# Kernel optimization log

Measured on AMD Instinct MI355X. Metric: run time of the kernel, lower is better.

## Reference

```python
import jax, jax.numpy as jnp
import numpy as np

NUM_HEADS = 8

def setup_inputs() -> dict:
    key = jax.random.key(0)
    ks = jax.random.split(key, 7)
    B, Cin, H, W = 4, 256, 56, 56
    Cout = 256
    s = 1.0 / np.sqrt(Cin)
    return {
        "x": jax.random.normal(ks[0], (B, Cin, H, W), dtype=jnp.float32),
        "wq": jax.random.normal(ks[1], (Cout, Cin), dtype=jnp.float32) * s,
        "bq": jax.random.normal(ks[2], (Cout,), dtype=jnp.float32) * s,
        "wk": jax.random.normal(ks[3], (Cout, Cin), dtype=jnp.float32) * s,
        "bk": jax.random.normal(ks[4], (Cout,), dtype=jnp.float32) * s,
        "wv": jax.random.normal(ks[5], (Cout, Cin), dtype=jnp.float32) * s,
        "bv": jax.random.normal(ks[6], (Cout,), dtype=jnp.float32) * s,
    }

def _proj(x, w, b):
    # 1x1 conv == per-pixel linear: [B,Cin,H,W] x [Cout,Cin] -> [B,Cout,H,W]
    return jnp.einsum('bchw,oc->bohw', x, w) + b[None, :, None, None]

def reference(x, wq, bq, wk, bk, wv, bv):
    B, _, H, W = x.shape
    Cout = wq.shape[0]
    hd = Cout // NUM_HEADS
    N = H * W
    # project and reshape to [B, heads, N, head_dim]
    def split_heads(t):
        return t.reshape(B, NUM_HEADS, hd, N).transpose(0, 1, 3, 2)
    q = split_heads(_proj(x, wq, bq))
    k = split_heads(_proj(x, wk, bk))
    v = split_heads(_proj(x, wv, bv))
    scores = jnp.einsum('bhnd,bhmd->bhnm', q, k) / jnp.sqrt(jnp.float32(hd))
    attn = jax.nn.softmax(scores, axis=-1)          # [B, heads, N, N]
    out = jnp.einsum('bhnm,bhmd->bhnd', attn, v)    # [B, heads, N, hd]
    out = out.transpose(0, 1, 3, 2).reshape(B, Cout, H, W)
    return out
```

## Files before the change

kernel.cpp:

```cpp
#include <hip/hip_runtime.h>
#include <math.h>


#define NB   4
#define CIN  256
#define NPIX 3136
#define NH   8
#define HD   32
#define QSC  0.25503837897544295f

typedef float          f32x4  __attribute__((ext_vector_type(4)));
typedef short          bf16x8 __attribute__((ext_vector_type(8)));
typedef unsigned int   u32x4  __attribute__((ext_vector_type(4)));
typedef unsigned int   u32x2  __attribute__((ext_vector_type(2)));
typedef unsigned short u16x4  __attribute__((ext_vector_type(4)));

static __device__ __forceinline__ unsigned short f2bf(float f) {
  union { float f; unsigned u; } v; v.f = f;
  return (unsigned short)((v.u + 0x7fffu + ((v.u >> 16) & 1u)) >> 16);
}

static __device__ __forceinline__ float fast_exp2(float x) {
#if __has_builtin(__builtin_amdgcn_exp2f)
  return __builtin_amdgcn_exp2f(x);
#else
  return exp2f(x);
#endif
}

static __device__ __forceinline__ unsigned cvt_pk_bf16(float lo, float hi) {
  unsigned r;
  asm("v_cvt_pk_bf16_f32 %0, %1, %2" : "=v"(r) : "v"(lo), "v"(hi));
  return r;
}

static __device__ __forceinline__ void gload_lds16(const void* g, void* l) {
  __builtin_amdgcn_global_load_lds(
      (__attribute__((address_space(1))) const void*)g,
      (__attribute__((address_space(3))) void*)l, 16, 0, 0);
}

static __device__ __forceinline__ bf16x8 lds_frag16(const unsigned char* p) {
  u32x4 u = *(const u32x4*)p;
  return __builtin_bit_cast(bf16x8, u);
}

__global__ __launch_bounds__(256) void k_xpose(const float* __restrict__ x,
                                               unsigned short* __restrict__ xbT) {
  __shared__ unsigned short tile[64][66];
  const int n0 = blockIdx.x * 64, c0 = blockIdx.y * 64, b = blockIdx.z;
  const int t = threadIdx.x;
  const int cl = t >> 4, nl = (t & 15) * 4;
#pragma unroll
  for (int rep = 0; rep < 4; ++rep) {
    const int c = cl + rep * 16;
    f32x4 v = *(const f32x4*)(x + ((size_t)(b * CIN + c0 + c)) * NPIX + n0 + nl);
    tile[nl + 0][c] = f2bf(v.x);
    tile[nl + 1][c] = f2bf(v.y);
    tile[nl + 2][c] = f2bf(v.z);
    tile[nl + 3][c] = f2bf(v.w);
  }
  __syncthreads();
  const int nr = t >> 2, co = (t & 3) * 16;
  unsigned pw[8];
#pragma unroll
  for (int j = 0; j < 8; ++j)
    pw[j] = (unsigned)tile[nr][co + 2 * j] | ((unsigned)tile[nr][co + 2 * j + 1] << 16);
  unsigned short* dst = xbT + ((size_t)(b * NPIX + n0 + nr)) * 256 + c0 + co;
  u32x4 lo = {pw[0], pw[1], pw[2], pw[3]};
  u32x4 hi = {pw[4], pw[5], pw[6], pw[7]};
  *(u32x4*)dst = lo;
  *(u32x4*)(dst + 8) = hi;
}

__global__ __launch_bounds__(256) void k_wconv(const float* __restrict__ wq,
                                               const float* __restrict__ wk,
                                               const float* __restrict__ wv,
                                               unsigned short* __restrict__ wb) {
  const int i = blockIdx.x * 256 + threadIdx.x;
  const int mat = i >> 16, idx = i & 65535;
  const float* w = (mat == 0) ? wq : (mat == 1 ? wk : wv);
  const float s = (mat == 0) ? QSC : 1.0f;
  wb[i] = f2bf(w[idx] * s);
}

__global__ __launch_bounds__(256) void k_proj(
    const unsigned short* __restrict__ xbT, const unsigned short* __restrict__ wb,
    const float* __restrict__ bq, const float* __restrict__ bk,
    const float* __restrict__ bv,
    unsigned short* __restrict__ qws, unsigned short* __restrict__ kws,
    unsigned short* __restrict__ vtws) {
  __shared__ alignas(16) unsigned char lds[20480];
  const int b = blockIdx.y & 3, mat = blockIdx.y >> 2;
  const int n0 = blockIdx.x * 64;
  const int t = threadIdx.x, l = t & 63, wid = t >> 6, g = l >> 4, q = l & 15;
  const unsigned short* wmat = wb + mat * (256 * 256);

  f32x4 acc[4][4] = {};

  for (int ks = 0; ks < 8; ++ks) {
#pragma unroll
    for (int r = 0; r < 4; ++r) {
      const unsigned short* src = wmat + ((wid + 4 * r) * 16 + q) * 256 + ks * 32 + g * 8;
      gload_lds16(src, lds + (r * 256 + t) * 16);
    }
    gload_lds16(xbT + ((size_t)(b * NPIX + n0 + wid * 16 + q)) * 256 + ks * 32 + g * 8,
                lds + 16384 + t * 16);
    __syncthreads();

    bf16x8 wa[4], xf[4];
#pragma unroll
    for (int r = 0; r < 4; ++r) wa[r] = lds_frag16(lds + (r * 256 + wid * 64 + l) * 16);
#pragma unroll
    for (int nt = 0; nt < 4; ++nt) xf[nt] = lds_frag16(lds + 16384 + (nt * 64 + l) * 16);
#pragma unroll
    for (int r = 0; r < 4; ++r)
#pragma unroll
      for (int nt = 0; nt < 4; ++nt)
        acc[r][nt] = __builtin_amdgcn_mfma_f32_16x16x32_bf16(wa[r], xf[nt], acc[r][nt], 0, 0, 0);
    __syncthreads();
  }

  const float* bias = (mat == 0) ? bq : (mat == 1 ? bk : bv);
  const float bsc = (mat == 0) ? QSC : 1.0f;
#pragma unroll
  for (int r = 0; r < 4; ++r) {
    const int ob = (wid + 4 * r) * 16 + g * 4;
    const int h = ob >> 5, d0 = ob & 31;
    const float b0 = bias[ob + 0] * bsc, b1 = bias[ob + 1] * bsc;
    const float b2 = bias[ob + 2] * bsc, b3 = bias[ob + 3] * bsc;
#pragma unroll
    for (int nt = 0; nt < 4; ++nt) {
      const int n = n0 + nt * 16 + q;
      f32x4 a = acc[r][nt];
      if (mat < 2) {
        unsigned short* dst = (mat == 0) ? qws : kws;
        u16x4 pk = {f2bf(a.x + b0), f2bf(a.y + b1), f2bf(a.z + b2), f2bf(a.w + b3)};
        *(u16x4*)(dst + ((size_t)((b * NH + h) * NPIX + n)) * HD + d0) = pk;
      } else {
        unsigned short* vr = vtws + ((size_t)((b * NH + h) * HD + d0)) * NPIX + n;
        vr[0] = f2bf(a.x + b0);
        vr[(size_t)NPIX] = f2bf(a.y + b1);
        vr[(size_t)2 * NPIX] = f2bf(a.z + b2);
        vr[(size_t)3 * NPIX] = f2bf(a.w + b3);
      }
    }
  }
}

__global__ __launch_bounds__(256) void k_attn(
    const unsigned short* __restrict__ qws, const unsigned short* __restrict__ kws,
    const unsigned short* __restrict__ vtws, float* __restrict__ out) {
  __shared__ alignas(16) unsigned char lds[24576];
  const int bh = blockIdx.y;
  const int q0 = blockIdx.x * 64;
  const int t = threadIdx.x, l = t & 63, wid = t >> 6, g = l >> 4, q = l & 15;

  u32x4 qu = *(const u32x4*)(qws + ((size_t)(bh * NPIX + q0 + wid * 16 + q)) * HD + g * 8);
  const bf16x8 qf = __builtin_bit_cast(bf16x8, qu);
  const f32x4 zero4 = {0.f, 0.f, 0.f, 0.f};

  float lsum = 0.0f;
  f32x4 oacc0 = zero4;
  f32x4 oacc1 = zero4;

  const unsigned short* ksrc = kws + ((size_t)(bh * NPIX + wid * 16 + q)) * HD + g * 8;
  const unsigned short* vsrc =
      vtws + ((size_t)(bh * HD + (wid >> 1) * 16 + q)) * NPIX + (wid & 1) * 32 + g * 8;

  unsigned bofs = 0;
  gload_lds16(ksrc, lds + t * 16);
  gload_lds16(vsrc, lds + 4096 + t * 16);
  __syncthreads();

  for (int kt = 0; kt < 49; ++kt) {
    if (kt < 48) {
      gload_lds16(ksrc + (size_t)(kt + 1) * 64 * HD, lds + (bofs ^ 8192) + t * 16);
      gload_lds16(vsrc + (kt + 1) * 64, lds + (bofs ^ 8192) + 4096 + t * 16);
    }
    const unsigned char* kb = lds + bofs;
    const unsigned char* vb = lds + bofs + 4096;

    f32x4 s[4];
#pragma unroll
    for (int jj = 0; jj < 4; ++jj) {
      bf16x8 kf = lds_frag16(kb + (jj * 64 + l) * 16);
      s[jj] = __builtin_amdgcn_mfma_f32_16x16x32_bf16(kf, qf, zero4, 0, 0, 0);
    }

    float psum = 0.0f;
    unsigned pw[8];
#pragma unroll
    for (int jj = 0; jj < 4; ++jj) {
#pragma unroll
      for (int rp = 0; rp < 2; ++rp) {
        float p0 = fast_exp2(s[jj][2 * rp + 0]);
        float p1 = fast_exp2(s[jj][2 * rp + 1]);
        psum += p0 + p1;
        pw[jj * 2 + rp] = cvt_pk_bf16(p0, p1);
      }
    }
    lsum += psum;

    {
      u32x4 c0 = {pw[0], pw[1], pw[2], pw[3]};
      u32x4 c1 = {pw[4], pw[5], pw[6], pw[7]};
      *(u32x4*)(lds + 16384 + wid * 2048 + l * 16) = c0;
      *(u32x4*)(lds + 16384 + wid * 2048 + 1024 + l * 16) = c1;
    }

#pragma unroll
    for (int c = 0; c < 2; ++c) {
      const unsigned char* pbase = lds + 16384 + wid * 2048 + c * 1024 + q * 16 + (g & 2) * 4;
      u32x2 plo = *(const u32x2*)(pbase + ((2 * g) & 3) * 256);
      u32x2 phi = *(const u32x2*)(pbase + ((2 * g + 1) & 3) * 256);
      u32x4 pu = {plo.x, plo.y, phi.x, phi.y};
      bf16x8 pf = __builtin_bit_cast(bf16x8, pu);
      bf16x8 v0 = lds_frag16(vb + (c * 64 + l) * 16);
      bf16x8 v1 = lds_frag16(vb + (128 + c * 64 + l) * 16);
      oacc0 = __builtin_amdgcn_mfma_f32_16x16x32_bf16(v0, pf, oacc0, 0, 0, 0);
      oacc1 = __builtin_amdgcn_mfma_f32_16x16x32_bf16(v1, pf, oacc1, 0, 0, 0);
    }

    __syncthreads();
    bofs ^= 8192;
  }

  lsum += __shfl_xor(lsum, 16, 64);
  lsum += __shfl_xor(lsum, 32, 64);
  const float inv = 1.0f / lsum;

  float* ob = out + (size_t)(bh * HD) * NPIX + q0 + wid * 16 + q;
#pragma unroll
  for (int r = 0; r < 4; ++r) {
    ob[(size_t)(g * 4 + r) * NPIX] = oacc0[r] * inv;
    ob[(size_t)(16 + g * 4 + r) * NPIX] = oacc1[r] * inv;
  }
}

extern "C" void kernel_launch(void* const* d_in, const int* in_sizes, int n_in,
                              void* d_out, int out_size, void* d_ws, size_t ws_size,
                              hipStream_t stream) {
  const float* x  = (const float*)d_in[0];
  const float* wq = (const float*)d_in[1];
  const float* bq = (const float*)d_in[2];
  const float* wk = (const float*)d_in[3];
  const float* bk = (const float*)d_in[4];
  const float* wv = (const float*)d_in[5];
  const float* bv = (const float*)d_in[6];
  float* out = (float*)d_out;

  unsigned char* ws = (unsigned char*)d_ws;
  unsigned short* xbT  = (unsigned short*)(ws);
  unsigned short* wb   = (unsigned short*)(ws + 6422528);
  unsigned short* qws  = (unsigned short*)(ws + 6815744);
  unsigned short* kws  = (unsigned short*)(ws + 13238272);
  unsigned short* vtws = (unsigned short*)(ws + 19660800);

  k_xpose<<<dim3(49, 4, 4), 256, 0, stream>>>(x, xbT);
  k_wconv<<<dim3(768), 256, 0, stream>>>(wq, wk, wv, wb);
  k_proj<<<dim3(49, 12), 256, 0, stream>>>(xbT, wb, bq, bk, bv, qws, kws, vtws);
  k_attn<<<dim3(49, 32), 256, 0, stream>>>(qws, kws, vtws, out);
}
```

Baseline: 117.4 us.

## Process two query tiles per wave to reuse K/V loads across 128 queries

Each attention block now handles 128 queries instead of 64, with each wave computing two 16-query tiles against the same K and V fragments loaded into LDS. This halves the K/V global-to-LDS traffic and per-tile synchronization relative to the compute, and the grid shrinks from 49 to 25 blocks per head. It also adds s_setprio around the MFMA groups and an explicit LDS wait plus scheduling barrier. The cost is more registers and LDS per block, fewer blocks (1.6k -> 800), and wasted work on the padded last tile, which relies on bounds checks.

```diff
diff --git a/kernel.cpp b/kernel.cpp
--- a/kernel.cpp
+++ b/kernel.cpp
@@ -151,22 +151,31 @@
 __global__ __launch_bounds__(256) void k_attn(
     const unsigned short* __restrict__ qws, const unsigned short* __restrict__ kws,
     const unsigned short* __restrict__ vtws, float* __restrict__ out) {
-  __shared__ alignas(16) unsigned char lds[24576];
+  __shared__ alignas(16) unsigned char lds[32768];
   const int bh = blockIdx.y;
-  const int q0 = blockIdx.x * 64;
+  const int q0 = blockIdx.x * 128;
   const int t = threadIdx.x, l = t & 63, wid = t >> 6, g = l >> 4, q = l & 15;
 
-  u32x4 qu = *(const u32x4*)(qws + ((size_t)(bh * NPIX + q0 + wid * 16 + q)) * HD + g * 8);
-  const bf16x8 qf = __builtin_bit_cast(bf16x8, qu);
+  const int nA = q0 + wid * 32 + q;
+  const int nB = nA + 16;
+  const int rowA = (nA < NPIX) ? nA : (NPIX - 1);
+  const int rowB = (nB < NPIX) ? nB : (NPIX - 1);
+
+  u32x4 quA = *(const u32x4*)(qws + ((size_t)(bh * NPIX + rowA)) * HD + g * 8);
+  u32x4 quB = *(const u32x4*)(qws + ((size_t)(bh * NPIX + rowB)) * HD + g * 8);
+  const bf16x8 qfA = __builtin_bit_cast(bf16x8, quA);
+  const bf16x8 qfB = __builtin_bit_cast(bf16x8, quB);
   const f32x4 zero4 = {0.f, 0.f, 0.f, 0.f};
 
-  float lsum = 0.0f;
-  f32x4 oacc0 = zero4;
-  f32x4 oacc1 = zero4;
+  float lsumA = 0.0f, lsumB = 0.0f;
+  f32x4 oA0 = zero4, oA1 = zero4, oB0 = zero4, oB1 = zero4;
 
   const unsigned short* ksrc = kws + ((size_t)(bh * NPIX + wid * 16 + q)) * HD + g * 8;
   const unsigned short* vsrc =
       vtws + ((size_t)(bh * HD + (wid >> 1) * 16 + q)) * NPIX + (wid & 1) * 32 + g * 8;
+
+  unsigned char* const pbaseA = lds + 16384 + wid * 4096;
+  unsigned char* const pbaseB = pbaseA + 2048;
 
   unsigned bofs = 0;
   gload_lds16(ksrc, lds + t * 16);
@@ -181,60 +190,109 @@
     const unsigned char* kb = lds + bofs;
     const unsigned char* vb = lds + bofs + 4096;
 
-    f32x4 s[4];
+    f32x4 sA[4], sB[4];
+    __builtin_amdgcn_s_setprio(1);
 #pragma unroll
     for (int jj = 0; jj < 4; ++jj) {
       bf16x8 kf = lds_frag16(kb + (jj * 64 + l) * 16);
-      s[jj] = __builtin_amdgcn_mfma_f32_16x16x32_bf16(kf, qf, zero4, 0, 0, 0);
-    }
-
-    float psum = 0.0f;
-    unsigned pw[8];
-#pragma unroll
-    for (int jj = 0; jj < 4; ++jj) {
-#pragma unroll
-      for (int rp = 0; rp < 2; ++rp) {
-        float p0 = fast_exp2(s[jj][2 * rp + 0]);
-        float p1 = fast_exp2(s[jj][2 * rp + 1]);
-        psum += p0 + p1;
-        pw[jj * 2 + rp] = cvt_pk_bf16(p0, p1);
+      sA[jj] = __builtin_amdgcn_mfma_f32_16x16x32_bf16(kf, qfA, zero4, 0, 0, 0);
+      sB[jj] = __builtin_amdgcn_mfma_f32_16x16x32_bf16(kf, qfB, zero4, 0, 0, 0);
+    }
+    __builtin_amdgcn_s_setprio(0);
+
+    {
+      float ps = 0.0f;
+      unsigned pw[8];
+#pragma unroll
+      for (int jj = 0; jj < 4; ++jj) {
+#pragma unroll
+        for (int rp = 0; rp < 2; ++rp) {
+          float p0 = fast_exp2(sA[jj][2 * rp + 0]);
+          float p1 = fast_exp2(sA[jj][2 * rp + 1]);
+          ps += p0 + p1;
+          pw[jj * 2 + rp] = cvt_pk_bf16(p0, p1);
+        }
       }
-    }
-    lsum += psum;
-
-    {
+      lsumA += ps;
       u32x4 c0 = {pw[0], pw[1], pw[2], pw[3]};
       u32x4 c1 = {pw[4], pw[5], pw[6], pw[7]};
-      *(u32x4*)(lds + 16384 + wid * 2048 + l * 16) = c0;
-      *(u32x4*)(lds + 16384 + wid * 2048 + 1024 + l * 16) = c1;
-    }
+      *(u32x4*)(pbaseA + l * 16) = c0;
+      *(u32x4*)(pbaseA + 1024 + l * 16) = c1;
+    }
+    {
+      float ps = 0.0f;
+      unsigned pw[8];
+#pragma unroll
+      for (int jj = 0; jj < 4; ++jj) {
+#pragma unroll
+        for (int rp = 0; rp < 2; ++rp) {
+          float p0 = fast_exp2(sB[jj][2 * rp + 0]);
+          float p1 = fast_exp2(sB[jj][2 * rp + 1]);
+          ps += p0 + p1;
+          pw[jj * 2 + rp] = cvt_pk_bf16(p0, p1);
+        }
+      }
+      lsumB += ps;
+      u32x4 c0 = {pw[0], pw[1], pw[2], pw[3]};
+      u32x4 c1 = {pw[4], pw[5], pw[6], pw[7]};
+      *(u32x4*)(pbaseB + l * 16) = c0;
+      *(u32x4*)(pbaseB + 1024 + l * 16) = c1;
+    }
+
+    asm volatile("s_waitcnt lgkmcnt(0)" ::: "memory");
+    __builtin_amdgcn_sched_barrier(0);
 
 #pragma unroll
     for (int c = 0; c < 2; ++c) {
-      const unsigned char* pbase = lds + 16384 + wid * 2048 + c * 1024 + q * 16 + (g & 2) * 4;
-      u32x2 plo = *(const u32x2*)(pbase + ((2 * g) & 3) * 256);
-      u32x2 phi = *(const u32x2*)(pbase + ((2 * g + 1) & 3) * 256);
-      u32x4 pu = {plo.x, plo.y, phi.x, phi.y};
-      bf16x8 pf = __builtin_bit_cast(bf16x8, pu);
       bf16x8 v0 = lds_frag16(vb + (c * 64 + l) * 16);
       bf16x8 v1 = lds_frag16(vb + (128 + c * 64 + l) * 16);
-      oacc0 = __builtin_amdgcn_mfma_f32_16x16x32_bf16(v0, pf, oacc0, 0, 0, 0);
-      oacc1 = __builtin_amdgcn_mfma_f32_16x16x32_bf16(v1, pf, oacc1, 0, 0, 0);
+
+      const unsigned char* pA = pbaseA + c * 1024 + q * 16 + (g & 2) * 4;
+      u32x2 alo = *(const u32x2*)(pA + ((2 * g) & 3) * 256);
+      u32x2 ahi = *(const u32x2*)(pA + ((2 * g + 1) & 3) * 256);
+      u32x4 au = {alo.x, alo.y, ahi.x, ahi.y};
+      bf16x8 pfA = __builtin_bit_cast(bf16x8, au);
+
+      const unsigned char* pB = pbaseB + c * 1024 + q * 16 + (g & 2) * 4;
+      u32x2 blo = *(const u32x2*)(pB + ((2 * g) & 3) * 256);
+      u32x2 bhi = *(const u32x2*)(pB + ((2 * g + 1) & 3) * 256);
+      u32x4 bu = {blo.x, blo.y, bhi.x, bhi.y};
+      bf16x8 pfB = __builtin_bit_cast(bf16x8, bu);
+
+      __builtin_amdgcn_s_setprio(1);
+      oA0 = __builtin_amdgcn_mfma_f32_16x16x32_bf16(v0, pfA, oA0, 0, 0, 0);
+      oA1 = __builtin_amdgcn_mfma_f32_16x16x32_bf16(v1, pfA, oA1, 0, 0, 0);
+      oB0 = __builtin_amdgcn_mfma_f32_16x16x32_bf16(v0, pfB, oB0, 0, 0, 0);
+      oB1 = __builtin_amdgcn_mfma_f32_16x16x32_bf16(v1, pfB, oB1, 0, 0, 0);
+      __builtin_amdgcn_s_setprio(0);
     }
 
     __syncthreads();
     bofs ^= 8192;
   }
 
-  lsum += __shfl_xor(lsum, 16, 64);
-  lsum += __shfl_xor(lsum, 32, 64);
-  const float inv = 1.0f / lsum;
-
-  float* ob = out + (size_t)(bh * HD) * NPIX + q0 + wid * 16 + q;
-#pragma unroll
-  for (int r = 0; r < 4; ++r) {
-    ob[(size_t)(g * 4 + r) * NPIX] = oacc0[r] * inv;
-    ob[(size_t)(16 + g * 4 + r) * NPIX] = oacc1[r] * inv;
+  lsumA += __shfl_xor(lsumA, 16, 64);
+  lsumA += __shfl_xor(lsumA, 32, 64);
+  lsumB += __shfl_xor(lsumB, 16, 64);
+  lsumB += __shfl_xor(lsumB, 32, 64);
+
+  if (nA < NPIX) {
+    const float inv = 1.0f / lsumA;
+    float* ob = out + (size_t)(bh * HD) * NPIX + nA;
+#pragma unroll
+    for (int r = 0; r < 4; ++r) {
+      ob[(size_t)(g * 4 + r) * NPIX] = oA0[r] * inv;
+      ob[(size_t)(16 + g * 4 + r) * NPIX] = oA1[r] * inv;
+    }
+  }
+  if (nB < NPIX) {
+    const float inv = 1.0f / lsumB;
+    float* ob = out + (size_t)(bh * HD) * NPIX + nB;
+#pragma unroll
+    for (int r = 0; r < 4; ++r) {
+      ob[(size_t)(g * 4 + r) * NPIX] = oB0[r] * inv;
+      ob[(size_t)(16 + g * 4 + r) * NPIX] = oB1[r] * inv;
+    }
   }
 }
 
@@ -260,5 +318,5 @@
   k_xpose<<<dim3(49, 4, 4), 256, 0, stream>>>(x, xbT);
   k_wconv<<<dim3(768), 256, 0, stream>>>(wq, wk, wv, wb);
   k_proj<<<dim3(49, 12), 256, 0, stream>>>(xbT, wb, bq, bk, bv, qws, kws, vtws);
-  k_attn<<<dim3(49, 32), 256, 0, stream>>>(qws, kws, vtws, out);
-}
+  k_attn<<<dim3(25, 32), 256, 0, stream>>>(qws, kws, vtws, out);
+}
```

Result: no change. 115.9 us (-1.3%).
